# Optimization experiments

Hardware: AMD Instinct MI355X
Metric: run time of the kernel (lower is better)

Reference implementation:

```python
import jax, jax.numpy as jnp
import numpy as np

B, Q, P, HID, H, KV, D = 2, 1024, 3072, 4096, 32, 8, 128
G = H // KV          # GQA group size
EPS = 1e-6
ROPE_THETA = 1e6


def setup_inputs() -> dict:
    key = jax.random.key(0)
    ks = jax.random.split(key, 8)
    hidden_states = jax.random.normal(ks[0], (B, Q, HID), jnp.float32)
    # real RoPE tables for positions [P, P+Q) (extend phase)
    pos = jnp.arange(P, P + Q, dtype=jnp.float32)
    inv_freq = 1.0 / (ROPE_THETA ** (jnp.arange(0, D, 2, dtype=jnp.float32) / D))
    freqs = pos[:, None] * inv_freq[None, :]            # [Q, D/2]
    emb = jnp.concatenate([freqs, freqs], axis=-1)       # [Q, D]
    cos = jnp.broadcast_to(jnp.cos(emb)[None], (B, Q, D)).astype(jnp.float32)
    sin = jnp.broadcast_to(jnp.sin(emb)[None], (B, Q, D)).astype(jnp.float32)
    k_cache = jax.random.normal(ks[1], (B, KV, P, D), jnp.float32)
    v_cache = jax.random.normal(ks[2], (B, KV, P, D), jnp.float32)
    s = 0.02
    Wq = jax.random.normal(ks[3], (HID, H * D), jnp.float32) * s
    Wk = jax.random.normal(ks[4], (HID, KV * D), jnp.float32) * s
    Wv = jax.random.normal(ks[5], (HID, KV * D), jnp.float32) * s
    Wo = jax.random.normal(ks[6], (H * D, HID), jnp.float32) * s
    q_norm_w = jnp.ones((D,), jnp.float32)
    k_norm_w = jnp.ones((D,), jnp.float32)
    return dict(hidden_states=hidden_states, cos=cos, sin=sin,
                k_cache=k_cache, v_cache=v_cache,
                Wq=Wq, Wk=Wk, Wv=Wv, Wo=Wo,
                q_norm_w=q_norm_w, k_norm_w=k_norm_w)


def _rmsnorm(x, w):
    var = jnp.mean(x * x, axis=-1, keepdims=True)
    return x * jax.lax.rsqrt(var + EPS) * w


def _rotate_half(x):
    x1, x2 = jnp.split(x, 2, axis=-1)
    return jnp.concatenate([-x2, x1], axis=-1)


def _rope(x, cos, sin):
    # x: [B, h, Q, D]; cos/sin: [B, Q, D] -> broadcast over heads
    c = cos[:, None, :, :]
    s = sin[:, None, :, :]
    return x * c + _rotate_half(x) * s


def reference(hidden_states, cos, sin, k_cache, v_cache,
              Wq, Wk, Wv, Wo, q_norm_w, k_norm_w):
    # projections
    q = (hidden_states @ Wq).reshape(B, Q, H, D)
    k = (hidden_states @ Wk).reshape(B, Q, KV, D)
    v = (hidden_states @ Wv).reshape(B, Q, KV, D)
    # per-head RMSNorm on q and k
    q = _rmsnorm(q, q_norm_w)
    k = _rmsnorm(k, k_norm_w)
    # [B, heads, Q, D]
    q = q.transpose(0, 2, 1, 3)
    k = k.transpose(0, 2, 1, 3)
    v = v.transpose(0, 2, 1, 3)
    q = _rope(q, cos, sin)
    k = _rope(k, cos, sin)
    # extend: concat cached prefix KV with new KV -> kv_len = P + Q
    K = jnp.concatenate([k_cache, k], axis=2)   # [B, KV, P+Q, D]
    V = jnp.concatenate([v_cache, v], axis=2)
    qg = q.reshape(B, KV, G, Q, D)
    scale = 1.0 / jnp.sqrt(jnp.float32(D))
    scores = jnp.einsum('bkgqd,bksd->bkgqs', qg, K) * scale  # [B,KV,G,Q,P+Q]
    # causal mask offset by prefix: query i sees keys <= P + i
    key_idx = jnp.arange(P + Q)
    mask = key_idx[None, :] <= (P + jnp.arange(Q))[:, None]  # [Q, P+Q]
    scores = jnp.where(mask[None, None, None], scores, jnp.float32(-1e30))
    attn = jax.nn.softmax(scores, axis=-1)
    out = jnp.einsum('bkgqs,bksd->bkgqd', attn, V)           # [B,KV,G,Q,D]
    out = out.reshape(B, H, Q, D).transpose(0, 2, 1, 3).reshape(B, Q, H * D)
    return out @ Wo
```

## Files before the change

kernel.cpp:

```cpp
#include <hip/hip_runtime.h>
#include <hip/hip_bf16.h>

#define B_ 2
#define Q_ 1024
#define P_ 3072
#define HID_ 4096
#define H_ 32
#define KV_ 8
#define D_ 128
#define S_ 4096
#define NQKV 6144
#define QSCALE 0.1275174432f

typedef __attribute__((ext_vector_type(4))) float f32x4;
typedef __attribute__((ext_vector_type(8))) unsigned short u16x8;
typedef __attribute__((ext_vector_type(4))) unsigned short u16x4;
typedef __attribute__((ext_vector_type(8))) __bf16 bf16x8;

__device__ __forceinline__ unsigned short f2bf(float f){
  unsigned u = __builtin_bit_cast(unsigned, f);
  unsigned r = (u + 0x7FFFu + ((u >> 16) & 1u)) >> 16;
  return (unsigned short)r;
}
__device__ __forceinline__ unsigned pk2bf(float lo, float hi){
  unsigned r;
  asm("v_cvt_pk_bf16_f32 %0, %1, %2" : "=v"(r) : "v"(lo), "v"(hi));
  return r;
}
__device__ __forceinline__ float fexp2(float x){
  float r; asm("v_exp_f32 %0, %1" : "=v"(r) : "v"(x)); return r;
}
__device__ __forceinline__ f32x4 mfma16(u16x8 a, u16x8 b, f32x4 c){
  return __builtin_amdgcn_mfma_f32_16x16x32_bf16(
      __builtin_bit_cast(bf16x8, a), __builtin_bit_cast(bf16x8, b), c, 0, 0, 0);
}
typedef const __attribute__((address_space(1))) void* gp1_t;
typedef __attribute__((address_space(3))) void* lp3_t;
__device__ __forceinline__ void gl16(const unsigned short* g, unsigned short* l){
  __builtin_amdgcn_global_load_lds((gp1_t)g, (lp3_t)l, 16, 0, 0);
}

#define N1_ 2097152
#define N2_ 1572864
__global__ __launch_bounds__(256) void setup(
    const float* __restrict__ hs, const float* __restrict__ kc,
    const float* __restrict__ vc, const float* __restrict__ qw,
    const float* __restrict__ kw, unsigned short* __restrict__ AH,
    unsigned short* __restrict__ Kb, unsigned short* __restrict__ VT,
    float* __restrict__ M){
  __shared__ unsigned short T[128][72];
  __shared__ float sa[4], sb[4];
  int bx = blockIdx.x;
  int tid = threadIdx.x;
  if(bx < 2048){
    const int PD = P_ * D_;
    const long SD = (long)S_ * D_;
    for(int i4 = bx * 256 + tid; i4 < N1_ + N2_; i4 += 2048 * 256){
      if(i4 < N1_){
        long i = (long)i4 * 4;
        float4 x = *(const float4*)(hs + i);
        *(u16x4*)(AH + i) = (u16x4){f2bf(x.x), f2bf(x.y), f2bf(x.z), f2bf(x.w)};
      } else {
        long i = (long)(i4 - N1_) * 4;
        int bkv = (int)(i / PD);
        int rem = (int)(i - (long)bkv * PD);
        long dst = (long)bkv * SD + rem;
        float4 k4 = *(const float4*)(kc + i);
        *(u16x4*)(Kb + dst) = (u16x4){f2bf(k4.x), f2bf(k4.y), f2bf(k4.z), f2bf(k4.w)};
      }
    }
  } else if(bx < 2816){
    int idx = bx - 2048;
    int bkv = idx / 48;
    int s0 = (idx % 48) * 64;
    int r = tid >> 2, dblk = (tid & 3) * 32;
    const float* src = vc + ((long)bkv * P_ + s0 + r) * 128 + dblk;
    #pragma unroll
    for(int u = 0; u < 8; ++u){
      float4 v = *(const float4*)(src + u*4);
      T[dblk + u*4 + 0][r] = f2bf(v.x);
      T[dblk + u*4 + 1][r] = f2bf(v.y);
      T[dblk + u*4 + 2][r] = f2bf(v.z);
      T[dblk + u*4 + 3][r] = f2bf(v.w);
    }
    __syncthreads();
    int d = tid >> 1, sh = (tid & 1) * 32;
    unsigned short* dst = VT + ((long)bkv * 128 + d) * S_ + s0 + sh;
    #pragma unroll
    for(int u = 0; u < 4; ++u){
      u16x8 v;
      #pragma unroll
      for(int j = 0; j < 8; ++j) v[j] = T[d][sh + u*8 + j];
      *(u16x8*)(dst + u*8) = v;
    }
  } else {
    float a = (tid < 128) ? fabsf(qw[tid]) : 0.f;
    float b = (tid < 128) ? fabsf(kw[tid]) : 0.f;
    #pragma unroll
    for(int o = 32; o; o >>= 1){
      a = fmaxf(a, __shfl_xor(a, o));
      b = fmaxf(b, __shfl_xor(b, o));
    }
    if((tid & 63) == 0){ sa[tid >> 6] = a; sb[tid >> 6] = b; }
    __syncthreads();
    if(tid == 0){
      float mq = fmaxf(fmaxf(sa[0], sa[1]), fmaxf(sa[2], sa[3]));
      float mk = fmaxf(fmaxf(sb[0], sb[1]), fmaxf(sb[2], sb[3]));
      M[0] = 128.0f * QSCALE * mq * mk * 1.01f + 0.25f;
    }
  }
}

__global__ __launch_bounds__(256) void convert_w(
    const float* __restrict__ Wq, const float* __restrict__ Wk,
    const float* __restrict__ Wv, const float* __restrict__ Wo,
    unsigned short* __restrict__ WT, unsigned short* __restrict__ WoT){
  __shared__ float tile[64][65];
  int x = blockIdx.x;
  const float* W; int ldn, n_off; unsigned short* dst; int n0;
  if(x < 64)      { W = Wq; ldn = 4096; n_off = 0;    dst = WT;  n0 = x * 64; }
  else if(x < 80) { W = Wk; ldn = 1024; n_off = 4096; dst = WT;  n0 = (x-64) * 64; }
  else if(x < 96) { W = Wv; ldn = 1024; n_off = 5120; dst = WT;  n0 = (x-80) * 64; }
  else            { W = Wo; ldn = 4096; n_off = 0;    dst = WoT; n0 = (x-96) * 64; }
  int k0 = blockIdx.y * 64;
  int tid = threadIdx.x;
  int r = tid >> 4, c = (tid & 15) * 4;
  #pragma unroll
  for(int j = 0; j < 4; ++j){
    float4 v = *(const float4*)(W + (long)(k0 + r + j*16) * ldn + n0 + c);
    tile[r + j*16][c] = v.x; tile[r + j*16][c+1] = v.y;
    tile[r + j*16][c+2] = v.z; tile[r + j*16][c+3] = v.w;
  }
  __syncthreads();
  #pragma unroll
  for(int j = 0; j < 4; ++j){
    int n = r + j*16;
    long o = (long)(n_off + n0 + n) * 4096 + k0 + c;
    *(u16x4*)(dst + o) = (u16x4){f2bf(tile[c][n]), f2bf(tile[c+1][n]),
                                 f2bf(tile[c+2][n]), f2bf(tile[c+3][n])};
  }
}

__global__ __launch_bounds__(256) void gemm_bf16(
    const unsigned short* __restrict__ Ag, const unsigned short* __restrict__ Bg,
    float* __restrict__ C, int nbx, int ldc){
  __shared__ __align__(16) unsigned short sA[4096], sB[4096];
  int tid = threadIdx.x;
  int nwg = nbx * 16;
  int lin = blockIdx.x;
  int cpx = nwg >> 3;
  int swz = (lin & 7) * cpx + (lin >> 3);
  int by = swz & 15, bx = swz >> 4;
  int m0 = by * 128, n0 = bx * 128;
  int lane = tid & 63, w = tid >> 6;
  int lr = lane & 15, lg = lane >> 4;
  int wm = (w >> 1) * 64, wn = (w & 1) * 64;
  int rowi = w * 16 + (lane >> 2);
  int cchunk = ((lane & 3) ^ ((lane >> 3) & 3)) << 3;
  const unsigned short* aP = Ag + (long)(m0 + rowi) * 4096 + cchunk;
  const unsigned short* bP = Bg + (long)(n0 + rowi) * 4096 + cchunk;
  const int step2 = 64 * 4096;
  unsigned short* dA = sA + w * 512;
  unsigned short* dB = sB + w * 512;
  int rdcol = (lg * 8) ^ (((lr >> 1) & 3) << 3);
  f32x4 zero = {0.f,0.f,0.f,0.f};
  f32x4 acc[4][4];
  #pragma unroll
  for(int mi=0;mi<4;++mi)
    #pragma unroll
    for(int ni=0;ni<4;++ni) acc[mi][ni] = zero;

  for(int kt = 0; kt < 128; ++kt){
    int kk = kt * 32;
    __syncthreads();
    gl16(aP + kk, dA);  gl16(aP + step2 + kk, dA + 2048);
    gl16(bP + kk, dB);  gl16(bP + step2 + kk, dB + 2048);
    __syncthreads();
    u16x8 ah[4];
    #pragma unroll
    for(int mi = 0; mi < 4; ++mi)
      ah[mi] = *(const u16x8*)(sA + (wm + mi*16 + lr) * 32 + rdcol);
    #pragma unroll
    for(int ni = 0; ni < 4; ++ni){
      u16x8 bh = *(const u16x8*)(sB + (wn + ni*16 + lr) * 32 + rdcol);
      #pragma unroll
      for(int mi = 0; mi < 4; ++mi)
        acc[mi][ni] = mfma16(ah[mi], bh, acc[mi][ni]);
    }
  }
  #pragma unroll
  for(int mi = 0; mi < 4; ++mi)
    #pragma unroll
    for(int r = 0; r < 4; ++r){
      long rowoff = (long)(m0 + wm + mi*16 + lg*4 + r) * ldc + n0 + wn + lr;
      #pragma unroll
      for(int ni = 0; ni < 4; ++ni)
        C[rowoff + ni*16] = acc[mi][ni][r];
    }
}

__global__ __launch_bounds__(256) void pp_qkv(
    const float* __restrict__ Craw, const float* __restrict__ cosb,
    const float* __restrict__ sinb, const float* __restrict__ qw,
    const float* __restrict__ kw, unsigned short* __restrict__ Qb,
    unsigned short* __restrict__ Kb, unsigned short* __restrict__ VT){
  int rid = blockIdx.x * 4 + (threadIdx.x >> 6);
  int lane = threadIdx.x & 63;
  if(rid < 65536){
    int b = rid >> 15;
    int rem = rid & 32767;
    int q = rem >> 5;
    int h = rem & 31;
    long rowoff = (long)(b * Q_ + q) * NQKV + h * 128;
    float x1 = Craw[rowoff + lane];
    float x2 = Craw[rowoff + 64 + lane];
    float ss = x1*x1 + x2*x2;
    for(int o = 32; o; o >>= 1) ss += __shfl_xor(ss, o);
    float norm = rsqrtf(ss * (1.0f/128.0f) + 1e-6f);
    float xn1 = x1 * norm * qw[lane];
    float xn2 = x2 * norm * qw[64 + lane];
    long co = (long)(b * Q_ + q) * 128;
    float c1 = cosb[co + lane],      s1 = sinb[co + lane];
    float c2 = cosb[co + 64 + lane], s2 = sinb[co + 64 + lane];
    float o1 = (xn1 * c1 - xn2 * s1) * QSCALE;
    float o2 = (xn2 * c2 + xn1 * s2) * QSCALE;
    long dst = ((long)(b * H_ + h) * Q_ + q) * 128;
    Qb[dst + lane] = f2bf(o1);
    Qb[dst + 64 + lane] = f2bf(o2);
  } else {
    int rid2 = rid - 65536;
    int b = rid2 >> 13;
    int rem = rid2 & 8191;
    int q = rem >> 3;
    int kv = rem & 7;
    int bkv = b * KV_ + kv;
    long rowoff = (long)(b * Q_ + q) * NQKV;
    float x1 = Craw[rowoff + 4096 + kv*128 + lane];
    float x2 = Craw[rowoff + 4096 + kv*128 + 64 + lane];
    float ss = x1*x1 + x2*x2;
    for(int o = 32; o; o >>= 1) ss += __shfl_xor(ss, o);
    float norm = rsqrtf(ss * (1.0f/128.0f) + 1e-6f);
    float xn1 = x1 * norm * kw[lane];
    float xn2 = x2 * norm * kw[64 + lane];
    long co = (long)(b * Q_ + q) * 128;
    float c1 = cosb[co + lane],      s1 = sinb[co + lane];
    float c2 = cosb[co + 64 + lane], s2 = sinb[co + 64 + lane];
    long dst = ((long)bkv * S_ + P_ + q) * 128;
    Kb[dst + lane]      = f2bf(xn1 * c1 - xn2 * s1);
    Kb[dst + 64 + lane] = f2bf(xn2 * c2 + xn1 * s2);
    float v1 = Craw[rowoff + 5120 + kv*128 + lane];
    float v2 = Craw[rowoff + 5120 + kv*128 + 64 + lane];
    VT[((long)bkv * 128 + lane) * S_ + P_ + q]      = f2bf(v1);
    VT[((long)bkv * 128 + 64 + lane) * S_ + P_ + q] = f2bf(v2);
  }
}

#define KVB 32
#define PSL 40
__global__ __launch_bounds__(256, 2) void attn(
    const unsigned short* __restrict__ Qg, const unsigned short* __restrict__ Kg,
    const unsigned short* __restrict__ VTg, const float* __restrict__ Mp,
    float* __restrict__ po, float* __restrict__ pl){
  __shared__ __align__(16) unsigned short Ks[2][KVB*128];
  __shared__ __align__(16) unsigned short Vs[2][128*KVB];
  __shared__ __align__(16) unsigned short Ps[4][64*PSL];
  int tid = threadIdx.x;
  int qb = blockIdx.x >> 1, sp = blockIdx.x & 1;
  int b = blockIdx.z, h = blockIdx.y, q0 = qb * 256;
  int kvh = h >> 2;
  int w = tid >> 6, lane = tid & 63, lr = lane & 15, lg = lane >> 4;
  int q0w = q0 + w * 64;
  float Mv = Mp[0];
  u16x8 qh[4][4];
  #pragma unroll
  for(int mi = 0; mi < 4; ++mi){
    long qbase = ((long)(b * H_ + h) * Q_ + q0w + mi*16 + lr) * 128;
    #pragma unroll
    for(int c = 0; c < 4; ++c)
      qh[mi][c] = *(const u16x8*)(Qg + qbase + c*32 + lg*8);
  }
  f32x4 minit = {-Mv, -Mv, -Mv, -Mv};
  f32x4 o[4][8];
  #pragma unroll
  for(int mi = 0; mi < 4; ++mi)
    #pragma unroll
    for(int i = 0; i < 8; ++i) o[mi][i] = (f32x4){0.f,0.f,0.f,0.f};
  float l[4] = {0.f, 0.f, 0.f, 0.f};
  long kb  = (long)(b * KV_ + kvh) * S_ * 128;
  long vb0 = (long)(b * KV_ + kvh) * 128 * (long)S_;
  int T = 104 + 8 * qb;
  int half = T >> 1;
  int t0 = sp ? half : 0;
  int t1 = sp ? T : half;
  int koff[2], voff[2], ldst[2];
  #pragma unroll
  for(int i = 0; i < 2; ++i){
    int L = (w*2 + i)*64 + lane;
    ldst[i] = L * 8;
    int r = L >> 4, c8 = (L & 15) ^ (r & 7);
    koff[i] = r*128 + c8*8;
    int d = ((L >> 3) << 1) | (L & 1);
    int sm = (L >> 1) & 3;
    int g = (d & 3) ^ ((d >> 2) & 3);
    voff[i] = d * S_ + ((sm ^ g) << 3);
  }
  {
    const unsigned short* kg = Kg + kb + (long)t0 * (KVB*128);
    const unsigned short* vg = VTg + vb0 + t0 * KVB;
    #pragma unroll
    for(int i = 0; i < 2; ++i){
      gl16(kg + koff[i], &Ks[t0 & 1][ldst[i]]);
      gl16(vg + voff[i], &Vs[t0 & 1][ldst[i]]);
    }
  }
  __syncthreads();

  int lr7 = lr & 7;
  int gread = (lr & 3) ^ ((lr >> 2) & 3);
  for(int t = t0; t < t1; ++t){
    int cur = t & 1;
    if(t + 1 < t1){
      int s1 = (t + 1) * KVB;
      const unsigned short* kg = Kg + kb + (long)s1 * 128;
      const unsigned short* vg = VTg + vb0 + s1;
      #pragma unroll
      for(int i = 0; i < 2; ++i){
        gl16(kg + koff[i], &Ks[cur^1][ldst[i]]);
        gl16(vg + voff[i], &Vs[cur^1][ldst[i]]);
      }
    }
    int s0 = t * KVB;
    if(s0 <= P_ + q0w + 63){
      f32x4 pacc[4][2];
      #pragma unroll
      for(int mi = 0; mi < 4; ++mi){ pacc[mi][0] = minit; pacc[mi][1] = minit; }
      __builtin_amdgcn_s_setprio(1);
      #pragma unroll
      for(int c = 0; c < 4; ++c)
        #pragma unroll
        for(int ni = 0; ni < 2; ++ni){
          u16x8 kh = *(const u16x8*)(&Ks[cur][(ni*16 + lr)*128 + (((c*4 + lg) ^ lr7) << 3)]);
          #pragma unroll
          for(int mi = 0; mi < 4; ++mi)
            pacc[mi][ni] = mfma16(kh, qh[mi][c], pacc[mi][ni]);
        }
      __builtin_amdgcn_s_setprio(0);
      if(s0 + KVB - 1 > P_ + q0w){
        #pragma unroll
        for(int mi = 0; mi < 4; ++mi){
          int qrow = q0w + mi*16 + lr;
          #pragma unroll
          for(int ni = 0; ni < 2; ++ni)
            #pragma unroll
            for(int r = 0; r < 4; ++r){
              int skey = s0 + ni*16 + lg*4 + r;
              if(skey > P_ + qrow) pacc[mi][ni][r] = -1e30f;
            }
        }
      }
      #pragma unroll
      for(int mi = 0; mi < 4; ++mi){
        float rs = 0.f;
        #pragma unroll
        for(int ni = 0; ni < 2; ++ni){
          float p0 = fexp2(pacc[mi][ni][0]);
          float p1 = fexp2(pacc[mi][ni][1]);
          float p2 = fexp2(pacc[mi][ni][2]);
          float p3 = fexp2(pacc[mi][ni][3]);
          rs += (p0 + p1) + (p2 + p3);
          uint2 pw; pw.x = pk2bf(p0, p1); pw.y = pk2bf(p2, p3);
          *(uint2*)(&Ps[w][(mi*16 + lr)*PSL + ni*16 + lg*4]) = pw;
        }
        l[mi] += rs;
      }
      u16x8 pa[4];
      #pragma unroll
      for(int mi = 0; mi < 4; ++mi)
        pa[mi] = *(const u16x8*)(&Ps[w][(mi*16 + lr)*PSL + lg*8]);
      __builtin_amdgcn_s_setprio(1);
      #pragma unroll
      for(int ni = 0; ni < 8; ++ni){
        int d = ni*16 + lr;
        int voffr = ((d >> 1) << 6) + ((lg ^ gread) << 4) + ((d & 1) << 3);
        u16x8 vbf = *(const u16x8*)(&Vs[cur][voffr]);
        #pragma unroll
        for(int mi = 0; mi < 4; ++mi)
          o[mi][ni] = mfma16(pa[mi], vbf, o[mi][ni]);
      }
      __builtin_amdgcn_s_setprio(0);
    }
    __syncthreads();
  }
  int bh = b * H_ + h;
  #pragma unroll
  for(int mi = 0; mi < 4; ++mi){
    float lt = l[mi];
    lt += __shfl_xor(lt, 16);
    lt += __shfl_xor(lt, 32);
    #pragma unroll
    for(int r = 0; r < 4; ++r){
      int qrow = q0w + mi*16 + lg*4 + r;
      long obase = ((long)(sp*64 + bh) * Q_ + qrow) * 128;
      #pragma unroll
      for(int ni = 0; ni < 8; ++ni)
        po[obase + ni*16 + lr] = o[mi][ni][r];
    }
    if(lane < 16)
      pl[(sp*64 + bh) * Q_ + q0w + mi*16 + lane] = lt;
  }
}

__global__ __launch_bounds__(256) void combine(
    const float* __restrict__ po, const float* __restrict__ pl,
    unsigned short* __restrict__ OH){
  int idx = blockIdx.x * 256 + threadIdx.x;
  int row = idx >> 5;
  int d4 = (idx & 31) * 4;
  int bh = row >> 10, q = row & 1023;
  int b = bh >> 5, h = bh & 31;
  float lsum = pl[bh*1024 + q] + pl[65536 + bh*1024 + q];
  float inv = 1.0f / lsum;
  float4 a = *(const float4*)(po + (long)row*128 + d4);
  float4 c = *(const float4*)(po + 8388608L + (long)row*128 + d4);
  u16x4 r = { f2bf((a.x + c.x) * inv), f2bf((a.y + c.y) * inv),
              f2bf((a.z + c.z) * inv), f2bf((a.w + c.w) * inv) };
  *(u16x4*)(OH + ((long)(b*1024 + q))*4096 + h*128 + d4) = r;
}

extern "C" void kernel_launch(void* const* d_in, const int* in_sizes, int n_in,
                              void* d_out, int out_size, void* d_ws, size_t ws_size,
                              hipStream_t stream){
  const float* hs   = (const float*)d_in[0];
  const float* cosb = (const float*)d_in[1];
  const float* sinb = (const float*)d_in[2];
  const float* kc   = (const float*)d_in[3];
  const float* vc   = (const float*)d_in[4];
  const float* Wq   = (const float*)d_in[5];
  const float* Wk   = (const float*)d_in[6];
  const float* Wv   = (const float*)d_in[7];
  const float* Wo   = (const float*)d_in[8];
  const float* qw   = (const float*)d_in[9];
  const float* kw   = (const float*)d_in[10];
  char* ws = (char*)d_ws;
  float* Craw          = (float*)ws;
  unsigned short* OH   = (unsigned short*)ws;
  unsigned short* WT   = (unsigned short*)(ws + 50331648);
  float* PO            = (float*)(ws + 50331648);
  unsigned short* WoT  = (unsigned short*)(ws + 117440512);
  unsigned short* AH   = (unsigned short*)(ws + 150994944);
  unsigned short* QB   = (unsigned short*)(ws + 150994944);
  unsigned short* KB   = (unsigned short*)(ws + 167772160);
  unsigned short* VT   = (unsigned short*)(ws + 184549376);
  float* PL            = (float*)(ws + 201326592);
  float* MW            = (float*)(ws + 201981952);
  float* Out = (float*)d_out;

  setup<<<dim3(2817), dim3(256), 0, stream>>>(hs, kc, vc, qw, kw, AH, KB, VT, MW);
  convert_w<<<dim3(160, 64), dim3(256), 0, stream>>>(Wq, Wk, Wv, Wo, WT, WoT);
  gemm_bf16<<<dim3(768), dim3(256), 0, stream>>>(AH, WT, Craw, 48, NQKV);
  pp_qkv<<<dim3(20480), dim3(256), 0, stream>>>(Craw, cosb, sinb, qw, kw, QB, KB, VT);
  attn<<<dim3(8, 32, 2), dim3(256), 0, stream>>>(QB, KB, VT, MW, PO, PL);
  combine<<<dim3(8192), dim3(256), 0, stream>>>(PO, PL, OH);
  gemm_bf16<<<dim3(512), dim3(256), 0, stream>>>(OH, WoT, Out, 32, 4096);
}
```

Before: 487.1 us.

## Fuse RMSNorm, RoPE and bf16 packing into the QKV GEMM epilogue

Replaces the separate pp_qkv pass with an epilogue inside a specialised QKV GEMM. Each 128-column tile maps to one head, so the epilogue transposes the tile through shared memory, applies the per-head RMSNorm and RoPE, and writes bf16 Q/K directly; V tiles are written transposed into VT. This removes the fp32 Craw round trip (a 48MB write plus read) and one launch, at the cost of extra LDS (about 33KB) and an epilogue that may lower occupancy. Workspace aliasing moves QB to the start of the buffer, overlapping OH.

Result: slower. 517.0 us (+6.1%).

```diff
diff --git a/kernel.cpp b/kernel.cpp
--- a/kernel.cpp
+++ b/kernel.cpp
@@ -141,6 +141,126 @@
   }
 }
 
+__global__ __launch_bounds__(256) void gemm_qkv(
+    const unsigned short* __restrict__ Ag, const unsigned short* __restrict__ Bg,
+    const float* __restrict__ cosb, const float* __restrict__ sinb,
+    const float* __restrict__ qw, const float* __restrict__ kw,
+    unsigned short* __restrict__ Qb, unsigned short* __restrict__ Kb,
+    unsigned short* __restrict__ VT){
+  __shared__ __align__(16) unsigned short sA[4096], sB[4096];
+  __shared__ float Tep[128][65];
+  int tid = threadIdx.x;
+  const int nbx = 48;
+  int nwg = nbx * 16;
+  int lin = blockIdx.x;
+  int cpx = nwg >> 3;
+  int swz = (lin & 7) * cpx + (lin >> 3);
+  int by = swz & 15, bx = swz >> 4;
+  int m0 = by * 128, n0 = bx * 128;
+  int lane = tid & 63, w = tid >> 6;
+  int lr = lane & 15, lg = lane >> 4;
+  int wm = (w >> 1) * 64, wn = (w & 1) * 64;
+  int rowi = w * 16 + (lane >> 2);
+  int cchunk = ((lane & 3) ^ ((lane >> 3) & 3)) << 3;
+  const unsigned short* aP = Ag + (long)(m0 + rowi) * 4096 + cchunk;
+  const unsigned short* bP = Bg + (long)(n0 + rowi) * 4096 + cchunk;
+  const int step2 = 64 * 4096;
+  unsigned short* dA = sA + w * 512;
+  unsigned short* dB = sB + w * 512;
+  int rdcol = (lg * 8) ^ (((lr >> 1) & 3) << 3);
+  f32x4 zero = {0.f,0.f,0.f,0.f};
+  f32x4 acc[4][4];
+  #pragma unroll
+  for(int mi=0;mi<4;++mi)
+    #pragma unroll
+    for(int ni=0;ni<4;++ni) acc[mi][ni] = zero;
+
+  for(int kt = 0; kt < 128; ++kt){
+    int kk = kt * 32;
+    __syncthreads();
+    gl16(aP + kk, dA);  gl16(aP + step2 + kk, dA + 2048);
+    gl16(bP + kk, dB);  gl16(bP + step2 + kk, dB + 2048);
+    __syncthreads();
+    u16x8 ah[4];
+    #pragma unroll
+    for(int mi = 0; mi < 4; ++mi)
+      ah[mi] = *(const u16x8*)(sA + (wm + mi*16 + lr) * 32 + rdcol);
+    #pragma unroll
+    for(int ni = 0; ni < 4; ++ni){
+      u16x8 bh = *(const u16x8*)(sB + (wn + ni*16 + lr) * 32 + rdcol);
+      #pragma unroll
+      for(int mi = 0; mi < 4; ++mi)
+        acc[mi][ni] = mfma16(ah[mi], bh, acc[mi][ni]);
+    }
+  }
+  if(bx >= 40){
+    int kv = bx - 40;
+    #pragma unroll
+    for(int mi = 0; mi < 4; ++mi){
+      int q0g = m0 + wm + mi*16 + lg*4;
+      int bb = q0g >> 10, qq = q0g & 1023;
+      #pragma unroll
+      for(int ni = 0; ni < 4; ++ni){
+        int d = wn + ni*16 + lr;
+        long dst = ((long)((bb*KV_ + kv)*128 + d))*S_ + P_ + qq;
+        u16x4 v = {f2bf(acc[mi][ni][0]), f2bf(acc[mi][ni][1]),
+                   f2bf(acc[mi][ni][2]), f2bf(acc[mi][ni][3])};
+        *(u16x4*)(VT + dst) = v;
+      }
+    }
+  } else {
+    int isQ = (bx < 32);
+    int h = isQ ? bx : (bx - 32);
+    const float* wv = isQ ? qw : kw;
+    float scale = isQ ? QSCALE : 1.0f;
+    #pragma unroll
+    for(int ch = 0; ch < 2; ++ch){
+      __syncthreads();
+      if((w >> 1) == ch){
+        #pragma unroll
+        for(int mi = 0; mi < 4; ++mi)
+          #pragma unroll
+          for(int ni = 0; ni < 4; ++ni){
+            int col = wn + ni*16 + lr;
+            int row0 = mi*16 + lg*4;
+            #pragma unroll
+            for(int r = 0; r < 4; ++r)
+              Tep[col][row0 + r] = acc[mi][ni][r];
+          }
+      }
+      __syncthreads();
+      #pragma unroll
+      for(int rr = 0; rr < 16; ++rr){
+        int row = w*16 + rr;
+        int grow = m0 + ch*64 + row;
+        int bb = grow >> 10, qq = grow & 1023;
+        float x1 = Tep[lane][row];
+        float x2 = Tep[64 + lane][row];
+        float ss = x1*x1 + x2*x2;
+        #pragma unroll
+        for(int of = 32; of; of >>= 1) ss += __shfl_xor(ss, of);
+        float norm = rsqrtf(ss * (1.0f/128.0f) + 1e-6f);
+        float xn1 = x1 * norm * wv[lane];
+        float xn2 = x2 * norm * wv[64 + lane];
+        long co = (long)(bb * Q_ + qq) * 128;
+        float c1 = cosb[co + lane],      s1 = sinb[co + lane];
+        float c2 = cosb[co + 64 + lane], s2 = sinb[co + 64 + lane];
+        float o1 = (xn1*c1 - xn2*s1) * scale;
+        float o2 = (xn2*c2 + xn1*s2) * scale;
+        if(isQ){
+          long dst = ((long)(bb*H_ + h)*Q_ + qq) * 128;
+          Qb[dst + lane] = f2bf(o1);
+          Qb[dst + 64 + lane] = f2bf(o2);
+        } else {
+          long dst = ((long)(bb*KV_ + h)*S_ + P_ + qq) * 128;
+          Kb[dst + lane] = f2bf(o1);
+          Kb[dst + 64 + lane] = f2bf(o2);
+        }
+      }
+    }
+  }
+}
+
 __global__ __launch_bounds__(256) void gemm_bf16(
     const unsigned short* __restrict__ Ag, const unsigned short* __restrict__ Bg,
     float* __restrict__ C, int nbx, int ldc){
@@ -199,62 +319,6 @@
     }
 }
 
-__global__ __launch_bounds__(256) void pp_qkv(
-    const float* __restrict__ Craw, const float* __restrict__ cosb,
-    const float* __restrict__ sinb, const float* __restrict__ qw,
-    const float* __restrict__ kw, unsigned short* __restrict__ Qb,
-    unsigned short* __restrict__ Kb, unsigned short* __restrict__ VT){
-  int rid = blockIdx.x * 4 + (threadIdx.x >> 6);
-  int lane = threadIdx.x & 63;
-  if(rid < 65536){
-    int b = rid >> 15;
-    int rem = rid & 32767;
-    int q = rem >> 5;
-    int h = rem & 31;
-    long rowoff = (long)(b * Q_ + q) * NQKV + h * 128;
-    float x1 = Craw[rowoff + lane];
-    float x2 = Craw[rowoff + 64 + lane];
-    float ss = x1*x1 + x2*x2;
-    for(int o = 32; o; o >>= 1) ss += __shfl_xor(ss, o);
-    float norm = rsqrtf(ss * (1.0f/128.0f) + 1e-6f);
-    float xn1 = x1 * norm * qw[lane];
-    float xn2 = x2 * norm * qw[64 + lane];
-    long co = (long)(b * Q_ + q) * 128;
-    float c1 = cosb[co + lane],      s1 = sinb[co + lane];
-    float c2 = cosb[co + 64 + lane], s2 = sinb[co + 64 + lane];
-    float o1 = (xn1 * c1 - xn2 * s1) * QSCALE;
-    float o2 = (xn2 * c2 + xn1 * s2) * QSCALE;
-    long dst = ((long)(b * H_ + h) * Q_ + q) * 128;
-    Qb[dst + lane] = f2bf(o1);
-    Qb[dst + 64 + lane] = f2bf(o2);
-  } else {
-    int rid2 = rid - 65536;
-    int b = rid2 >> 13;
-    int rem = rid2 & 8191;
-    int q = rem >> 3;
-    int kv = rem & 7;
-    int bkv = b * KV_ + kv;
-    long rowoff = (long)(b * Q_ + q) * NQKV;
-    float x1 = Craw[rowoff + 4096 + kv*128 + lane];
-    float x2 = Craw[rowoff + 4096 + kv*128 + 64 + lane];
-    float ss = x1*x1 + x2*x2;
-    for(int o = 32; o; o >>= 1) ss += __shfl_xor(ss, o);
-    float norm = rsqrtf(ss * (1.0f/128.0f) + 1e-6f);
-    float xn1 = x1 * norm * kw[lane];
-    float xn2 = x2 * norm * kw[64 + lane];
-    long co = (long)(b * Q_ + q) * 128;
-    float c1 = cosb[co + lane],      s1 = sinb[co + lane];
-    float c2 = cosb[co + 64 + lane], s2 = sinb[co + 64 + lane];
-    long dst = ((long)bkv * S_ + P_ + q) * 128;
-    Kb[dst + lane]      = f2bf(xn1 * c1 - xn2 * s1);
-    Kb[dst + 64 + lane] = f2bf(xn2 * c2 + xn1 * s2);
-    float v1 = Craw[rowoff + 5120 + kv*128 + lane];
-    float v2 = Craw[rowoff + 5120 + kv*128 + 64 + lane];
-    VT[((long)bkv * 128 + lane) * S_ + P_ + q]      = f2bf(v1);
-    VT[((long)bkv * 128 + 64 + lane) * S_ + P_ + q] = f2bf(v2);
-  }
-}
-
 #define KVB 32
 #define PSL 40
 __global__ __launch_bounds__(256, 2) void attn(
@@ -442,13 +506,12 @@
   const float* qw   = (const float*)d_in[9];
   const float* kw   = (const float*)d_in[10];
   char* ws = (char*)d_ws;
-  float* Craw          = (float*)ws;
+  unsigned short* QB   = (unsigned short*)ws;
   unsigned short* OH   = (unsigned short*)ws;
   unsigned short* WT   = (unsigned short*)(ws + 50331648);
   float* PO            = (float*)(ws + 50331648);
   unsigned short* WoT  = (unsigned short*)(ws + 117440512);
   unsigned short* AH   = (unsigned short*)(ws + 150994944);
-  unsigned short* QB   = (unsigned short*)(ws + 150994944);
   unsigned short* KB   = (unsigned short*)(ws + 167772160);
   unsigned short* VT   = (unsigned short*)(ws + 184549376);
   float* PL            = (float*)(ws + 201326592);
@@ -457,8 +520,7 @@
 
   setup<<<dim3(2817), dim3(256), 0, stream>>>(hs, kc, vc, qw, kw, AH, KB, VT, MW);
   convert_w<<<dim3(160, 64), dim3(256), 0, stream>>>(Wq, Wk, Wv, Wo, WT, WoT);
-  gemm_bf16<<<dim3(768), dim3(256), 0, stream>>>(AH, WT, Craw, 48, NQKV);
-  pp_qkv<<<dim3(20480), dim3(256), 0, stream>>>(Craw, cosb, sinb, qw, kw, QB, KB, VT);
+  gemm_qkv<<<dim3(768), dim3(256), 0, stream>>>(AH, WT, cosb, sinb, qw, kw, QB, KB, VT);
   attn<<<dim3(8, 32, 2), dim3(256), 0, stream>>>(QB, KB, VT, MW, PO, PL);
   combine<<<dim3(8192), dim3(256), 0, stream>>>(PO, PL, OH);
   gemm_bf16<<<dim3(512), dim3(256), 0, stream>>>(OH, WoT, Out, 32, 4096);
```
